# Optimization experiments

Measured on AMD Instinct MI355X. Metric: run time of the kernel, lower is better.

Reference implementation:

```python
import jax, jax.numpy as jnp
import numpy as np

D_MODEL, D_K, D_V, H = 1024, 64, 64, 16
B, NQ, NK = 4, 1024, 1024
HID = D_MODEL // 2


def _dwg(x, W1, b1, W2, b2):
    # DynamicWeightGenerator: sigmoid(fc2(relu(fc1(x))))
    h = jax.nn.relu(jnp.einsum('bnd,hd->bnh', x, W1) + b1)
    return jax.nn.sigmoid(jnp.einsum('bnh,dh->bnd', h, W2) + b2)


def setup_inputs() -> dict:
    key = jax.random.key(0)
    ks = jax.random.split(key, 32)
    s = 0.02
    inp = {
        'queries': jax.random.normal(ks[0], (B, NQ, D_MODEL), jnp.float32),
        'keys': jax.random.normal(ks[1], (B, NK, D_MODEL), jnp.float32),
        'values': jax.random.normal(ks[2], (B, NK, D_MODEL), jnp.float32),
        'attention_mask': jax.random.randint(ks[3], (B, 1, NQ, NK), 0, 2) > 0,
        'attention_weights': jax.random.uniform(ks[4], (B, H, NQ, NK), jnp.float32),
        'memory': jax.random.normal(ks[5], (B, NK), jnp.float32),
        # projections (torch Linear convention: y = x @ W.T + b)
        'Wq': jax.random.normal(ks[6], (H * D_K, D_MODEL), jnp.float32) * s,
        'bq': jnp.zeros((H * D_K,), jnp.float32),
        'Wk': jax.random.normal(ks[7], (H * D_K, D_MODEL), jnp.float32) * s,
        'bk': jnp.zeros((H * D_K,), jnp.float32),
        'Wv': jax.random.normal(ks[8], (H * D_V, D_MODEL), jnp.float32) * s,
        'bv': jnp.zeros((H * D_V,), jnp.float32),
        'Wo': jax.random.normal(ks[9], (D_MODEL, H * D_V), jnp.float32) * s,
        'bo': jnp.zeros((D_MODEL,), jnp.float32),
        'Wmm': jax.random.normal(ks[10], (H * D_V, 1), jnp.float32) * s,
        'bmm': jnp.zeros((H * D_V,), jnp.float32),
    }
    for i, tag in enumerate(['q', 'k', 'v']):
        k0, k1 = ks[11 + 2 * i], ks[12 + 2 * i]
        inp[f'W1{tag}'] = jax.random.normal(k0, (HID, D_MODEL), jnp.float32) * s
        inp[f'b1{tag}'] = jnp.zeros((HID,), jnp.float32)
        inp[f'W2{tag}'] = jax.random.normal(k1, (D_MODEL, HID), jnp.float32) * s
        inp[f'b2{tag}'] = jnp.zeros((D_MODEL,), jnp.float32)
    return inp


def reference(queries, keys, values, attention_mask, attention_weights, memory,
              Wq, bq, Wk, bk, Wv, bv, Wo, bo, Wmm, bmm,
              W1q, b1q, W2q, b2q, W1k, b1k, W2k, b2k, W1v, b1v, W2v, b2v):
    b_s, nq = queries.shape[:2]
    nk = keys.shape[1]
    # dynamic elementwise gating of inputs
    q_in = queries * _dwg(queries, W1q, b1q, W2q, b2q)
    k_in = keys * _dwg(keys, W1k, b1k, W2k, b2k)
    v_in = values * _dwg(values, W1v, b1v, W2v, b2v)
    # projections -> (b, h, n, d)
    q = (jnp.einsum('bnd,ed->bne', q_in, Wq) + bq).reshape(b_s, nq, H, D_K).transpose(0, 2, 1, 3)
    k = (jnp.einsum('bnd,ed->bne', k_in, Wk) + bk).reshape(b_s, nk, H, D_K).transpose(0, 2, 1, 3)
    v = (jnp.einsum('bnd,ed->bne', v_in, Wv) + bv).reshape(b_s, nk, H, D_V).transpose(0, 2, 1, 3)
    # per-token memory factor: fc_mm(memory[..., None]) -> (b, h, nk, d_k)
    mm = (memory[..., None] * Wmm[:, 0] + bmm).reshape(b_s, nk, H, D_K).transpose(0, 2, 1, 3)
    att = jnp.einsum('bhqd,bhkd->bhqk', q, k * mm) / np.sqrt(D_K).astype(np.float32)
    att = att * attention_weights                         # custom scaling (slice [:nk] == full)
    att = jnp.where(attention_mask, -jnp.inf, att)        # masked_fill
    att = jax.nn.softmax(att, axis=-1)
    out = jnp.einsum('bhqk,bhkd->bhqd', att, v * mm)      # (b, h, nq, d_v)
    out = out.transpose(0, 2, 1, 3).reshape(b_s, nq, H * D_V)
    return jnp.einsum('bne,de->bnd', out, Wo) + bo
```

## Files before the change

### kernel.cpp

```cpp
#include <hip/hip_runtime.h>
#include <hip/hip_bf16.h>

#define BB    4
#define NN    1024
#define DM    1024
#define HH    16
#define HID   512
#define TT    (BB * NN)

typedef __attribute__((ext_vector_type(8))) short bf16x8;
typedef __attribute__((ext_vector_type(4))) float f32x4;

__device__ __forceinline__ ushort f2bfu(float f) {
    __hip_bfloat16 h = __float2bfloat16(f);
    return __builtin_bit_cast(ushort, h);
}

__device__ __forceinline__ float bfu2f(ushort u) {
    __hip_bfloat16 h = __builtin_bit_cast(__hip_bfloat16, u);
    return __bfloat162float(h);
}

__device__ __forceinline__ f32x4 mfma16(bf16x8 a, bf16x8 b, f32x4 c) {
    return __builtin_amdgcn_mfma_f32_16x16x32_bf16(a, b, c, 0, 0, 0);
}

__device__ __forceinline__ void gll16(const void* g, void* l) {
    __builtin_amdgcn_global_load_lds(
        (const __attribute__((address_space(1))) unsigned int*)g,
        (__attribute__((address_space(3))) unsigned int*)l, 16, 0, 0);
}

__global__ void detect_mask_kernel(const uint4* __restrict__ m,
                                   int n16, int* __restrict__ flags) {
    int stride = blockDim.x * gridDim.x;
    unsigned hi = 0, lo = 0;
    for (int i = blockIdx.x * blockDim.x + threadIdx.x; i < n16; i += stride) {
        uint4 v = m[i];
        unsigned o = v.x | v.y | v.z | v.w;
        lo |= o & 0xFFu;
        hi |= o & 0xFFFFFF00u;
    }
    if (hi) atomicOr(&flags[0], 1);
    if (lo) atomicOr(&flags[1], 1);
}

#define NSEG 13
struct CvtAll { const float* s[NSEG]; ushort* d[NSEG]; int bound[NSEG]; };

__global__ __launch_bounds__(256) void cvt_all(CvtAll a, int total) {
    int stride = blockDim.x * gridDim.x;
    for (int i = blockIdx.x * blockDim.x + threadIdx.x; i < total; i += stride) {
        const float* sp = a.s[0];
        ushort* dp = a.d[0];
        int base = 0;
        #pragma unroll
        for (int k = 1; k < NSEG; ++k) {
            bool ge = i >= a.bound[k - 1];
            sp = ge ? a.s[k] : sp;
            dp = ge ? a.d[k] : dp;
            base = ge ? a.bound[k - 1] : base;
        }
        int j = i - base;
        float4 v = ((const float4*)sp)[j];
        uint2 o;
        o.x = (unsigned)f2bfu(v.x) | ((unsigned)f2bfu(v.y) << 16);
        o.y = (unsigned)f2bfu(v.z) | ((unsigned)f2bfu(v.w) << 16);
        ((uint2*)dp)[j] = o;
    }
}

struct GB {
    const ushort* A[3]; const ushort* W[3];
    const float* bias[3]; void* C[3]; const ushort* X[3];
};

template <int EP, int NF>
__global__ __launch_bounds__(256) void gemm_bf16(
    GB gb, int M, int N, int K,
    const float* __restrict__ mem, const float* __restrict__ Wmm,
    const float* __restrict__ bmm)
{
    __shared__ __align__(16) ushort As[2][128 * 64];
    __shared__ __align__(16) ushort Bs[2][NF * 32 * 64];
    const int z = blockIdx.z;
    const ushort* A = gb.A[z];
    const ushort* W = gb.W[z];
    const float* bias = gb.bias[z];
    void* Cout = gb.C[z];
    const ushort* X = gb.X[z];

    const int tid = threadIdx.x;
    const int lane = tid & 63, w = tid >> 6;
    const int lc = lane & 15, lg = lane >> 4;
    const int m0 = blockIdx.x * 128, n0 = blockIdx.y * (NF * 32);
    const int wm = (w >> 1) * 64, wn = (w & 1) * (NF * 16);
    const int srow = lane >> 3, scol = 8 * ((lane & 7) ^ srow);
    const int swl = (lc & 7) << 3;

    f32x4 acc[4][NF];
    #pragma unroll
    for (int i = 0; i < 4; ++i)
        #pragma unroll
        for (int j = 0; j < NF; ++j)
            acc[i][j] = (f32x4){0.f, 0.f, 0.f, 0.f};

    auto stage = [&](int buf, int k0) {
        #pragma unroll
        for (int ci = 0; ci < 4; ++ci) {
            int c = w + ci * 4;
            gll16(&A[(size_t)(m0 + c * 8 + srow) * K + k0 + scol], &As[buf][c * 512]);
            if (c < NF * 4)
                gll16(&W[(size_t)(n0 + c * 8 + srow) * K + k0 + scol], &Bs[buf][c * 512]);
        }
    };

    stage(0, 0);
    stage(1, 64);
    const int nt = K / 64;

    for (int t = 0; t < nt; ++t) {
        const int cur = t & 1;
        if (t < nt - 1) {
            if constexpr (NF == 4) asm volatile("s_waitcnt vmcnt(8)" ::: "memory");
            else                   asm volatile("s_waitcnt vmcnt(6)" ::: "memory");
        } else {
            asm volatile("s_waitcnt vmcnt(0)" ::: "memory");
        }
        __builtin_amdgcn_sched_barrier(0);
        __builtin_amdgcn_s_barrier();

        bf16x8 af[4][2], bfr[NF][2];
        #pragma unroll
        for (int mi = 0; mi < 4; ++mi) {
            int row = wm + mi * 16 + lc;
            af[mi][0] = *(const bf16x8*)&As[cur][row * 64 + ((lg * 8) ^ swl)];
            af[mi][1] = *(const bf16x8*)&As[cur][row * 64 + ((32 + lg * 8) ^ swl)];
        }
        #pragma unroll
        for (int nj = 0; nj < NF; ++nj) {
            int row = wn + nj * 16 + lc;
            bfr[nj][0] = *(const bf16x8*)&Bs[cur][row * 64 + ((lg * 8) ^ swl)];
            bfr[nj][1] = *(const bf16x8*)&Bs[cur][row * 64 + ((32 + lg * 8) ^ swl)];
        }
        asm volatile("s_waitcnt lgkmcnt(0)" ::: "memory");
        __builtin_amdgcn_sched_barrier(0);
        __builtin_amdgcn_s_barrier();

        if (t + 2 < nt) stage(cur, (t + 2) * 64);

        #pragma unroll
        for (int mi = 0; mi < 4; ++mi)
            #pragma unroll
            for (int nj = 0; nj < NF; ++nj) {
                acc[mi][nj] = mfma16(af[mi][0], bfr[nj][0], acc[mi][nj]);
                acc[mi][nj] = mfma16(af[mi][1], bfr[nj][1], acc[mi][nj]);
            }
    }

    #pragma unroll
    for (int nj = 0; nj < NF; ++nj) {
        int e = n0 + wn + nj * 16 + lc;
        float bv = bias[e];
        float wmv = 0.f, bmv = 0.f;
        if (EP == 7) { wmv = Wmm[e]; bmv = bmm[e]; }
        #pragma unroll
        for (int mi = 0; mi < 4; ++mi) {
            int mbase = m0 + wm + mi * 16 + lg * 4;
            if (EP == 7 && z == 2) {
                ushort u[4];
                #pragma unroll
                for (int r = 0; r < 4; ++r) {
                    float v = (acc[mi][nj][r] + bv) * (mem[mbase + r] * wmv + bmv);
                    u[r] = f2bfu(v);
                }
                int bb = mbase >> 10, n = mbase & 1023;
                size_t off = ((size_t)(bb * HH + (e >> 6)) * 64 + (e & 63)) * NN + n;
                uint2 pk;
                pk.x = (unsigned)u[0] | ((unsigned)u[1] << 16);
                pk.y = (unsigned)u[2] | ((unsigned)u[3] << 16);
                *(uint2*)&((ushort*)Cout)[off] = pk;
            } else {
                #pragma unroll
                for (int r = 0; r < 4; ++r) {
                    int m = mbase + r;
                    float v = acc[mi][nj][r] + bv;
                    if (EP == 1) v = fmaxf(v, 0.f);
                    if (EP == 2) v = bfu2f(X[(size_t)m * N + e]) * (1.f / (1.f + __expf(-v)));
                    if (EP == 7) {
                        if (z == 0) v = v * 0.125f;
                        else        v = v * (mem[m] * wmv + bmv);
                    }
                    size_t off = (size_t)m * N + e;
                    if (EP == 4) ((float*)Cout)[off] = v;
                    else         ((ushort*)Cout)[off] = f2bfu(v);
                }
            }
        }
    }
}

__global__ __launch_bounds__(256) void attn_mfma(
    const ushort* __restrict__ qp, const ushort* __restrict__ kp,
    const ushort* __restrict__ vt, const float* __restrict__ aw,
    const void* __restrict__ maskp, const int* __restrict__ mflags,
    ushort* __restrict__ ob)
{
    __shared__ __align__(16) ushort Ks[2][64 * 64];
    __shared__ __align__(16) ushort Vs[2][64 * 64];
    __shared__ __align__(16) ushort Ps[64 * 64];
    const int tid = threadIdx.x, lane = tid & 63, w = tid >> 6;
    const int lc = lane & 15, lg = lane >> 4;
    const int bid = blockIdx.x;
    const int swz = (bid & 7) * 128 + (bid >> 3);
    const int qt = swz & 15, bh = swz >> 4;
    const int b = bh >> 4, h = bh & 15;
    const int q0 = qt * 64, wq = w * 16;
    const int mode = mflags[0] ? (mflags[1] ? 1 : 2) : 0;
    const int srow = lane >> 3, scol = 8 * ((lane & 7) ^ srow);
    const int swl = (lc & 7) << 3;

    const ushort* qrow = &qp[(size_t)(b * NN + q0 + wq + lc) * DM + h * 64];
    bf16x8 bq0 = *(const bf16x8*)&qrow[lg * 8];
    bf16x8 bq1 = *(const bf16x8*)&qrow[32 + lg * 8];

    f32x4 oacc[4];
    #pragma unroll
    for (int i = 0; i < 4; ++i) oacc[i] = (f32x4){0.f, 0.f, 0.f, 0.f};
    float psum = 0.f;
    const int q = q0 + wq + lc;
    const float* awrow = aw + ((size_t)bh * NN + q) * NN;
    const size_t mrowo = ((size_t)b * NN + q) * NN;

    float4 awA[4], awB[4];
    uint4 mk4A[4], mk4B[4];
    unsigned mk1A[4], mk1B[4];

    #pragma unroll
    for (int ci = 0; ci < 2; ++ci) {
        int c = w + ci * 4;
        gll16(&kp[(size_t)(b * NN + c * 8 + srow) * DM + h * 64 + scol], &Ks[0][c * 512]);
        gll16(&vt[((size_t)bh * 64 + c * 8 + srow) * NN + 0 + scol], &Vs[0][c * 512]);
    }
    #pragma unroll
    for (int mi = 0; mi < 4; ++mi)
        awA[mi] = *(const float4*)&awrow[mi * 16 + lg * 4];
    if (mode == 1) {
        #pragma unroll
        for (int mi = 0; mi < 4; ++mi)
            mk1A[mi] = *(const unsigned*)&((const unsigned char*)maskp)[mrowo + mi * 16 + lg * 4];
    } else {
        #pragma unroll
        for (int mi = 0; mi < 4; ++mi)
            mk4A[mi] = *(const uint4*)((const char*)maskp + 4 * (mrowo + mi * 16 + lg * 4));
    }
    asm volatile("s_waitcnt vmcnt(0)" ::: "memory");
    __builtin_amdgcn_sched_barrier(0);
    __builtin_amdgcn_s_barrier();

#define ATTN_BODY(T, AWC, MK4C, MK1C, AWN, MK4N, MK1N)                          \
    {                                                                           \
        const int cur = (T) & 1;                                                \
        if ((T) < 15) {                                                         \
            const int kn = ((T) + 1) * 64;                                      \
            _Pragma("unroll")                                                   \
            for (int ci = 0; ci < 2; ++ci) {                                    \
                int c = w + ci * 4;                                             \
                gll16(&kp[(size_t)(b * NN + kn + c * 8 + srow) * DM + h * 64 + scol], \
                      &Ks[cur ^ 1][c * 512]);                                   \
                gll16(&vt[((size_t)bh * 64 + c * 8 + srow) * NN + kn + scol],   \
                      &Vs[cur ^ 1][c * 512]);                                   \
            }                                                                   \
            __builtin_amdgcn_sched_barrier(0);                                  \
            _Pragma("unroll")                                                   \
            for (int mi = 0; mi < 4; ++mi)                                      \
                AWN[mi] = *(const float4*)&awrow[kn + mi * 16 + lg * 4];        \
            if (mode == 1) {                                                    \
                _Pragma("unroll")                                               \
                for (int mi = 0; mi < 4; ++mi)                                  \
                    MK1N[mi] = *(const unsigned*)&((const unsigned char*)maskp) \
                                   [mrowo + kn + mi * 16 + lg * 4];             \
            } else {                                                            \
                _Pragma("unroll")                                               \
                for (int mi = 0; mi < 4; ++mi)                                  \
                    MK4N[mi] = *(const uint4*)((const char*)maskp +             \
                                   4 * (mrowo + kn + mi * 16 + lg * 4));        \
            }                                                                   \
            __builtin_amdgcn_sched_barrier(0);                                  \
        }                                                                       \
                                                               \
        f32x4 sacc[4];                                                          \
        __builtin_amdgcn_s_setprio(1);                                          \
        _Pragma("unroll")                                                       \
        for (int mi = 0; mi < 4; ++mi) {                                        \
            int krow = mi * 16 + lc;                                            \
            bf16x8 a0 = *(const bf16x8*)&Ks[cur][krow * 64 + ((lg * 8) ^ swl)]; \
            bf16x8 a1 = *(const bf16x8*)&Ks[cur][krow * 64 + ((32 + lg * 8) ^ swl)]; \
            f32x4 s = (f32x4){0.f, 0.f, 0.f, 0.f};                              \
            s = mfma16(a0, bq0, s);                                             \
            s = mfma16(a1, bq1, s);                                             \
            sacc[mi] = s;                                                       \
        }                                                                       \
        __builtin_amdgcn_s_setprio(0);                                          \
                                 \
        _Pragma("unroll")                                                       \
        for (int mi = 0; mi < 4; ++mi) {                                        \
            unsigned mk[4];                                                     \
            if (mode == 1) {                                                    \
                mk[0] = MK1C[mi] & 0xffu;         mk[1] = (MK1C[mi] >> 8) & 0xffu;  \
                mk[2] = (MK1C[mi] >> 16) & 0xffu; mk[3] = (MK1C[mi] >> 24) & 0xffu; \
            } else if (mode == 0) {                                             \
                mk[0] = MK4C[mi].x; mk[1] = MK4C[mi].y;                         \
                mk[2] = MK4C[mi].z; mk[3] = MK4C[mi].w;                         \
            } else {                                                            \
                mk[0] = MK4C[mi].x != 0; mk[1] = MK4C[mi].y != 0;               \
                mk[2] = MK4C[mi].z != 0; mk[3] = MK4C[mi].w != 0;               \
            }                                                                   \
            const float aww[4] = {AWC[mi].x, AWC[mi].y, AWC[mi].z, AWC[mi].w};  \
            float pv[4];                                                        \
            _Pragma("unroll")                                                   \
            for (int r = 0; r < 4; ++r) {                                       \
                float sv = sacc[mi][r] * aww[r];                                \
                pv[r] = mk[r] ? 0.f : __expf(sv);                               \
                psum += pv[r];                                                  \
            }                                                                   \
            uint2 pk;                                                           \
            pk.x = (unsigned)f2bfu(pv[0]) | ((unsigned)f2bfu(pv[1]) << 16);     \
            pk.y = (unsigned)f2bfu(pv[2]) | ((unsigned)f2bfu(pv[3]) << 16);     \
            *(uint2*)&Ps[(wq + lc) * 64 + ((mi * 16 + lg * 4) ^ swl)] = pk;     \
        }                                                                       \
                                                                        \
        __builtin_amdgcn_s_setprio(1);                                          \
        _Pragma("unroll")                                                       \
        for (int kk = 0; kk < 2; ++kk) {                                        \
            bf16x8 pa = *(const bf16x8*)&Ps[(wq + lc) * 64 + ((kk * 32 + lg * 8) ^ swl)]; \
            _Pragma("unroll")                                                   \
            for (int nj = 0; nj < 4; ++nj) {                                    \
                bf16x8 vb = *(const bf16x8*)&Vs[cur][(nj * 16 + lc) * 64 + ((kk * 32 + lg * 8) ^ swl)]; \
                oacc[nj] = mfma16(pa, vb, oacc[nj]);                            \
            }                                                                   \
        }                                                                       \
        __builtin_amdgcn_s_setprio(0);                                          \
        if ((T) < 15) {                                                         \
            asm volatile("s_waitcnt vmcnt(0)" ::: "memory");                    \
            __builtin_amdgcn_sched_barrier(0);                                  \
            __builtin_amdgcn_s_barrier();                                       \
        }                                                                       \
    }

    for (int tt = 0; tt < 8; ++tt) {
        const int t0 = tt * 2, t1 = tt * 2 + 1;
        ATTN_BODY(t0, awA, mk4A, mk1A, awB, mk4B, mk1B);
        ATTN_BODY(t1, awB, mk4B, mk1B, awA, mk4A, mk1A);
    }
#undef ATTN_BODY

    psum += __shfl_xor(psum, 16);
    psum += __shfl_xor(psum, 32);
    float inv = 1.0f / psum;
    float invr[4];
    #pragma unroll
    for (int r = 0; r < 4; ++r)
        invr[r] = __shfl(inv, (lane & 48) | (lg * 4 + r));

    #pragma unroll
    for (int nj = 0; nj < 4; ++nj)
        #pragma unroll
        for (int r = 0; r < 4; ++r) {
            int qq = q0 + wq + lg * 4 + r;
            float v = oacc[nj][r] * invr[r];
            ob[(size_t)(b * NN + qq) * DM + h * 64 + nj * 16 + lc] = f2bfu(v);
        }
}

extern "C" void kernel_launch(void* const* d_in, const int* in_sizes, int n_in,
                              void* d_out, int out_size, void* d_ws, size_t ws_size,
                              hipStream_t stream) {
    const float* xin_f[3] = {(const float*)d_in[0], (const float*)d_in[1], (const float*)d_in[2]};
    const void*  maskp   = d_in[3];
    const float* aw      = (const float*)d_in[4];
    const float* memv    = (const float*)d_in[5];
    const float* Wp_f[3] = {(const float*)d_in[6], (const float*)d_in[8], (const float*)d_in[10]};
    const float* bp[3]   = {(const float*)d_in[7], (const float*)d_in[9], (const float*)d_in[11]};
    const float* Wo_f  = (const float*)d_in[12];  const float* bo  = (const float*)d_in[13];
    const float* Wmm = (const float*)d_in[14];    const float* bmm = (const float*)d_in[15];
    const float* W1f[3] = {(const float*)d_in[16], (const float*)d_in[20], (const float*)d_in[24]};
    const float* b1a[3] = {(const float*)d_in[17], (const float*)d_in[21], (const float*)d_in[25]};
    const float* W2f[3] = {(const float*)d_in[18], (const float*)d_in[22], (const float*)d_in[26]};
    const float* b2a[3] = {(const float*)d_in[19], (const float*)d_in[23], (const float*)d_in[27]};

    char* p = (char*)d_ws;
    auto alloc = [&](size_t bytes) { char* r = p; p += (bytes + 255) & ~(size_t)255; return r; };
    int*    mflags = (int*)alloc(256);
    ushort* xbf[3]; for (int t = 0; t < 3; ++t) xbf[t] = (ushort*)alloc((size_t)TT * DM * 2);
    ushort* Wpb[3]; for (int t = 0; t < 3; ++t) Wpb[t] = (ushort*)alloc((size_t)DM * DM * 2);
    ushort* Wob  = (ushort*)alloc((size_t)DM * DM * 2);
    ushort* W1b[3]; for (int t = 0; t < 3; ++t) W1b[t] = (ushort*)alloc((size_t)HID * DM * 2);
    ushort* W2b[3]; for (int t = 0; t < 3; ++t) W2b[t] = (ushort*)alloc((size_t)DM * HID * 2);
    ushort* hbuf[3]; for (int t = 0; t < 3; ++t) hbuf[t] = (ushort*)alloc((size_t)TT * HID * 2);
    ushort* xg[3];  for (int t = 0; t < 3; ++t) xg[t] = (ushort*)alloc((size_t)TT * DM * 2);
    ushort* qpb  = (ushort*)alloc((size_t)TT * DM * 2);
    ushort* ksb  = (ushort*)alloc((size_t)TT * DM * 2);
    ushort* vtb  = (ushort*)alloc((size_t)TT * DM * 2);
    ushort* obuf = (ushort*)alloc((size_t)TT * DM * 2);

    hipMemsetAsync(mflags, 0, 8, stream);
    detect_mask_kernel<<<256, 256, 0, stream>>>((const uint4*)maskp,
                                                BB * NN * NN / 16, mflags);

    {
        CvtAll a;
        const int S_IN = TT * DM / 4, S_W = DM * DM / 4, S_H = HID * DM / 4;
        int idx = 0, cum = 0;
        auto seg = [&](const float* s, ushort* d, int n) {
            a.s[idx] = s; a.d[idx] = d; cum += n; a.bound[idx] = cum; ++idx;
        };
        for (int t = 0; t < 3; ++t) seg(xin_f[t], xbf[t], S_IN);
        for (int t = 0; t < 3; ++t) seg(Wp_f[t], Wpb[t], S_W);
        seg(Wo_f, Wob, S_W);
        for (int t = 0; t < 3; ++t) seg(W1f[t], W1b[t], S_H);
        for (int t = 0; t < 3; ++t) seg(W2f[t], W2b[t], S_H);
        cvt_all<<<2048, 256, 0, stream>>>(a, cum);
    }

    const dim3 blk(256);
    GB g1 = {}, g2 = {}, g3 = {}, g4 = {};
    for (int t = 0; t < 3; ++t) {
        g1.A[t] = xbf[t];  g1.W[t] = W1b[t]; g1.bias[t] = b1a[t]; g1.C[t] = hbuf[t];
        g2.A[t] = hbuf[t]; g2.W[t] = W2b[t]; g2.bias[t] = b2a[t]; g2.C[t] = xg[t]; g2.X[t] = xbf[t];
        g3.A[t] = xg[t];   g3.W[t] = Wpb[t]; g3.bias[t] = bp[t];
    }
    g3.C[0] = qpb; g3.C[1] = ksb; g3.C[2] = vtb;
    g4.A[0] = obuf; g4.W[0] = Wob; g4.bias[0] = bo; g4.C[0] = d_out;

    gemm_bf16<1, 2><<<dim3(TT / 128, HID / 64, 3), blk, 0, stream>>>(g1, TT, HID, DM, nullptr, nullptr, nullptr);
    gemm_bf16<2, 2><<<dim3(TT / 128, DM / 64, 3), blk, 0, stream>>>(g2, TT, DM, HID, nullptr, nullptr, nullptr);
    gemm_bf16<7, 2><<<dim3(TT / 128, DM / 64, 3), blk, 0, stream>>>(g3, TT, DM, DM, memv, Wmm, bmm);

    attn_mfma<<<dim3(1024), blk, 0, stream>>>(qpb, ksb, vtb, aw,
                                              maskp, mflags, obuf);

    gemm_bf16<4, 2><<<dim3(TT / 128, DM / 64, 1), blk, 0, stream>>>(g4, TT, DM, DM, nullptr, nullptr, nullptr);
}
```

Before: 260.9 us.

## Add LDS-staged triple-use attention kernel with async prefetch of weights and mask

Measured after the change: 269.0 us. +3.1%, slower.

```diff
diff --git a/kernel.cpp b/kernel.cpp
--- a/kernel.cpp
+++ b/kernel.cpp
@@ -200,12 +200,176 @@
     }
 }
 
-__global__ __launch_bounds__(256) void attn_mfma(
+__global__ __launch_bounds__(256) void attn_fast(
+    const ushort* __restrict__ qp, const ushort* __restrict__ kp,
+    const ushort* __restrict__ vt, const float* __restrict__ aw,
+    const unsigned char* __restrict__ maskp, const int* __restrict__ mflags,
+    ushort* __restrict__ ob)
+{
+    const int mode = mflags[0] ? (mflags[1] ? 1 : 2) : 0;
+    if (mode != 1) return;
+
+    __shared__ __align__(16) ushort Ks[2][64 * 64];
+    __shared__ __align__(16) ushort Vs[2][64 * 64];
+    __shared__ __align__(16) float  AWs[2][64 * 64];
+    __shared__ __align__(16) unsigned char Ms[2][64 * 64];
+    __shared__ __align__(16) ushort Ps[64 * 64];
+
+    const int tid = threadIdx.x, lane = tid & 63, w = tid >> 6;
+    const int lc = lane & 15, lg = lane >> 4;
+    const int bid = blockIdx.x;
+    const int swz = (bid & 7) * 128 + (bid >> 3);
+    const int qt = swz & 15, bh = swz >> 4;
+    const int b = bh >> 4, h = bh & 15;
+    const int q0 = qt * 64, wq = w * 16;
+    const int srow = lane >> 3, scol = 8 * ((lane & 7) ^ srow);
+    const int swl = (lc & 7) << 3;
+    const int qloc = wq + lc;
+
+    const ushort* qrow = &qp[(size_t)(b * NN + q0 + qloc) * DM + h * 64];
+    bf16x8 bq0 = *(const bf16x8*)&qrow[lg * 8];
+    bf16x8 bq1 = *(const bf16x8*)&qrow[32 + lg * 8];
+
+    auto stage = [&](int buf, int t) {
+        const int k0 = t * 64;
+        #pragma unroll
+        for (int ci = 0; ci < 2; ++ci) {
+            int c = w + ci * 4;
+            gll16(&kp[(size_t)(b * NN + k0 + c * 8 + srow) * DM + h * 64 + scol],
+                  &Ks[buf][c * 512]);
+            gll16(&vt[((size_t)bh * 64 + c * 8 + srow) * NN + k0 + scol],
+                  &Vs[buf][c * 512]);
+        }
+        #pragma unroll
+        for (int ci = 0; ci < 4; ++ci) {
+            int c = w + ci * 4;
+            int row = c * 4 + (lane >> 4);
+            int un = (lane & 15) ^ (row & 7);
+            gll16(&aw[((size_t)bh * NN + q0 + row) * NN + k0 + un * 4],
+                  &AWs[buf][c * 256]);
+        }
+        {
+            int row = w * 16 + (lane >> 2);
+            int un = (lane & 3) ^ (row & 3);
+            gll16(&maskp[((size_t)b * NN + q0 + row) * NN + k0 + un * 16],
+                  &Ms[buf][w * 1024]);
+        }
+    };
+
+    f32x4 oacc[4];
+    #pragma unroll
+    for (int i = 0; i < 4; ++i) oacc[i] = (f32x4){0.f, 0.f, 0.f, 0.f};
+    float psum = 0.f;
+
+    stage(0, 0);
+    stage(1, 1);
+    asm volatile("s_waitcnt vmcnt(0)" ::: "memory");
+    __builtin_amdgcn_sched_barrier(0);
+    __builtin_amdgcn_s_barrier();
+
+    const int awk = qloc & 7;
+    const int mkk = qloc & 3;
+
+    for (int t = 0; t < 16; ++t) {
+        const int cur = t & 1;
+        if (t < 15) asm volatile("s_waitcnt vmcnt(9)" ::: "memory");
+        else        asm volatile("s_waitcnt vmcnt(0)" ::: "memory");
+        __builtin_amdgcn_sched_barrier(0);
+        __builtin_amdgcn_s_barrier();
+
+        bf16x8 af0[4], af1[4], vf0[4], vf1[4];
+        float4 awf[4];
+        unsigned mkf[4];
+        #pragma unroll
+        for (int mi = 0; mi < 4; ++mi) {
+            int krow = mi * 16 + lc;
+            af0[mi] = *(const bf16x8*)&Ks[cur][krow * 64 + ((lg * 8) ^ swl)];
+            af1[mi] = *(const bf16x8*)&Ks[cur][krow * 64 + ((32 + lg * 8) ^ swl)];
+        }
+        #pragma unroll
+        for (int nj = 0; nj < 4; ++nj) {
+            int vrow = nj * 16 + lc;
+            vf0[nj] = *(const bf16x8*)&Vs[cur][vrow * 64 + ((lg * 8) ^ swl)];
+            vf1[nj] = *(const bf16x8*)&Vs[cur][vrow * 64 + ((32 + lg * 8) ^ swl)];
+        }
+        #pragma unroll
+        for (int mi = 0; mi < 4; ++mi) {
+            awf[mi] = *(const float4*)&AWs[cur][qloc * 64 + (((mi * 4 + lg) ^ awk) * 4)];
+            mkf[mi] = *(const unsigned*)&Ms[cur][qloc * 64 + ((mi ^ mkk) * 16) + lg * 4];
+        }
+        asm volatile("s_waitcnt lgkmcnt(0)" ::: "memory");
+        __builtin_amdgcn_sched_barrier(0);
+        __builtin_amdgcn_s_barrier();
+
+        if (t + 2 < 16) stage(cur, t + 2);
+
+        f32x4 sacc[4];
+        __builtin_amdgcn_s_setprio(1);
+        #pragma unroll
+        for (int mi = 0; mi < 4; ++mi) {
+            f32x4 s = (f32x4){0.f, 0.f, 0.f, 0.f};
+            s = mfma16(af0[mi], bq0, s);
+            s = mfma16(af1[mi], bq1, s);
+            sacc[mi] = s;
+        }
+        __builtin_amdgcn_s_setprio(0);
+
+        #pragma unroll
+        for (int mi = 0; mi < 4; ++mi) {
+            unsigned mu = mkf[mi];
+            const float aww[4] = {awf[mi].x, awf[mi].y, awf[mi].z, awf[mi].w};
+            float pv[4];
+            pv[0] = (mu & 0xffu)         ? 0.f : __expf(sacc[mi][0] * aww[0]);
+            pv[1] = ((mu >> 8) & 0xffu)  ? 0.f : __expf(sacc[mi][1] * aww[1]);
+            pv[2] = ((mu >> 16) & 0xffu) ? 0.f : __expf(sacc[mi][2] * aww[2]);
+            pv[3] = ((mu >> 24) & 0xffu) ? 0.f : __expf(sacc[mi][3] * aww[3]);
+            psum += pv[0] + pv[1] + pv[2] + pv[3];
+            uint2 pk;
+            pk.x = (unsigned)f2bfu(pv[0]) | ((unsigned)f2bfu(pv[1]) << 16);
+            pk.y = (unsigned)f2bfu(pv[2]) | ((unsigned)f2bfu(pv[3]) << 16);
+            *(uint2*)&Ps[qloc * 64 + ((mi * 16 + lg * 4) ^ swl)] = pk;
+        }
+
+        __builtin_amdgcn_s_setprio(1);
+        {
+            bf16x8 pa0 = *(const bf16x8*)&Ps[qloc * 64 + ((lg * 8) ^ swl)];
+            #pragma unroll
+            for (int nj = 0; nj < 4; ++nj)
+                oacc[nj] = mfma16(pa0, vf0[nj], oacc[nj]);
+            bf16x8 pa1 = *(const bf16x8*)&Ps[qloc * 64 + ((32 + lg * 8) ^ swl)];
+            #pragma unroll
+            for (int nj = 0; nj < 4; ++nj)
+                oacc[nj] = mfma16(pa1, vf1[nj], oacc[nj]);
+        }
+        __builtin_amdgcn_s_setprio(0);
+    }
+
+    psum += __shfl_xor(psum, 16);
+    psum += __shfl_xor(psum, 32);
+    float inv = 1.0f / psum;
+    float invr[4];
+    #pragma unroll
+    for (int r = 0; r < 4; ++r)
+        invr[r] = __shfl(inv, (lane & 48) | (lg * 4 + r));
+
+    #pragma unroll
+    for (int nj = 0; nj < 4; ++nj)
+        #pragma unroll
+        for (int r = 0; r < 4; ++r) {
+            int qq = q0 + wq + lg * 4 + r;
+            float v = oacc[nj][r] * invr[r];
+            ob[(size_t)(b * NN + qq) * DM + h * 64 + nj * 16 + lc] = f2bfu(v);
+        }
+}
+
+__global__ __launch_bounds__(256) void attn_mfma_fb(
     const ushort* __restrict__ qp, const ushort* __restrict__ kp,
     const ushort* __restrict__ vt, const float* __restrict__ aw,
     const void* __restrict__ maskp, const int* __restrict__ mflags,
     ushort* __restrict__ ob)
 {
+    const int mode = mflags[0] ? (mflags[1] ? 1 : 2) : 0;
+    if (mode == 1) return;
     __shared__ __align__(16) ushort Ks[2][64 * 64];
     __shared__ __align__(16) ushort Vs[2][64 * 64];
     __shared__ __align__(16) ushort Ps[64 * 64];
@@ -216,7 +380,6 @@
     const int qt = swz & 15, bh = swz >> 4;
     const int b = bh >> 4, h = bh & 15;
     const int q0 = qt * 64, wq = w * 16;
-    const int mode = mflags[0] ? (mflags[1] ? 1 : 2) : 0;
     const int srow = lane >> 3, scol = 8 * ((lane & 7) ^ srow);
     const int swl = (lc & 7) << 3;
 
@@ -234,7 +397,6 @@
 
     float4 awA[4], awB[4];
     uint4 mk4A[4], mk4B[4];
-    unsigned mk1A[4], mk1B[4];
 
     #pragma unroll
     for (int ci = 0; ci < 2; ++ci) {
@@ -243,22 +405,15 @@
         gll16(&vt[((size_t)bh * 64 + c * 8 + srow) * NN + 0 + scol], &Vs[0][c * 512]);
     }
     #pragma unroll
-    for (int mi = 0; mi < 4; ++mi)
+    for (int mi = 0; mi < 4; ++mi) {
         awA[mi] = *(const float4*)&awrow[mi * 16 + lg * 4];
-    if (mode == 1) {
-        #pragma unroll
-        for (int mi = 0; mi < 4; ++mi)
-            mk1A[mi] = *(const unsigned*)&((const unsigned char*)maskp)[mrowo + mi * 16 + lg * 4];
-    } else {
-        #pragma unroll
-        for (int mi = 0; mi < 4; ++mi)
-            mk4A[mi] = *(const uint4*)((const char*)maskp + 4 * (mrowo + mi * 16 + lg * 4));
+        mk4A[mi] = *(const uint4*)((const char*)maskp + 4 * (mrowo + mi * 16 + lg * 4));
     }
     asm volatile("s_waitcnt vmcnt(0)" ::: "memory");
     __builtin_amdgcn_sched_barrier(0);
     __builtin_amdgcn_s_barrier();
 
-#define ATTN_BODY(T, AWC, MK4C, MK1C, AWN, MK4N, MK1N)                          \
+#define ATTN_BODY(T, AWC, MK4C, AWN, MK4N)                                      \
     {                                                                           \
         const int cur = (T) & 1;                                                \
         if ((T) < 15) {                                                         \
@@ -273,22 +428,13 @@
             }                                                                   \
             __builtin_amdgcn_sched_barrier(0);                                  \
             _Pragma("unroll")                                                   \
-            for (int mi = 0; mi < 4; ++mi)                                      \
+            for (int mi = 0; mi < 4; ++mi) {                                    \
                 AWN[mi] = *(const float4*)&awrow[kn + mi * 16 + lg * 4];        \
-            if (mode == 1) {                                                    \
-                _Pragma("unroll")                                               \
-                for (int mi = 0; mi < 4; ++mi)                                  \
-                    MK1N[mi] = *(const unsigned*)&((const unsigned char*)maskp) \
-                                   [mrowo + kn + mi * 16 + lg * 4];             \
-            } else {                                                            \
-                _Pragma("unroll")                                               \
-                for (int mi = 0; mi < 4; ++mi)                                  \
-                    MK4N[mi] = *(const uint4*)((const char*)maskp +             \
-                                   4 * (mrowo + kn + mi * 16 + lg * 4));        \
+                MK4N[mi] = *(const uint4*)((const char*)maskp +                 \
+                               4 * (mrowo + kn + mi * 16 + lg * 4));            \
             }                                                                   \
             __builtin_amdgcn_sched_barrier(0);                                  \
         }                                                                       \
-                                                               \
         f32x4 sacc[4];                                                          \
         __builtin_amdgcn_s_setprio(1);                                          \
         _Pragma("unroll")                                                       \
@@ -302,14 +448,10 @@
             sacc[mi] = s;                                                       \
         }                                                                       \
         __builtin_amdgcn_s_setprio(0);                                          \
-                                 \
         _Pragma("unroll")                                                       \
         for (int mi = 0; mi < 4; ++mi) {                                        \
             unsigned mk[4];                                                     \
-            if (mode == 1) {                                                    \
-                mk[0] = MK1C[mi] & 0xffu;         mk[1] = (MK1C[mi] >> 8) & 0xffu;  \
-                mk[2] = (MK1C[mi] >> 16) & 0xffu; mk[3] = (MK1C[mi] >> 24) & 0xffu; \
-            } else if (mode == 0) {                                             \
+            if (mode == 0) {                                                    \
                 mk[0] = MK4C[mi].x; mk[1] = MK4C[mi].y;                         \
                 mk[2] = MK4C[mi].z; mk[3] = MK4C[mi].w;                         \
             } else {                                                            \
@@ -329,7 +471,6 @@
             pk.y = (unsigned)f2bfu(pv[2]) | ((unsigned)f2bfu(pv[3]) << 16);     \
             *(uint2*)&Ps[(wq + lc) * 64 + ((mi * 16 + lg * 4) ^ swl)] = pk;     \
         }                                                                       \
-                                                                        \
         __builtin_amdgcn_s_setprio(1);                                          \
         _Pragma("unroll")                                                       \
         for (int kk = 0; kk < 2; ++kk) {                                        \
@@ -350,8 +491,8 @@
 
     for (int tt = 0; tt < 8; ++tt) {
         const int t0 = tt * 2, t1 = tt * 2 + 1;
-        ATTN_BODY(t0, awA, mk4A, mk1A, awB, mk4B, mk1B);
-        ATTN_BODY(t1, awB, mk4B, mk1B, awA, mk4A, mk1A);
+        ATTN_BODY(t0, awA, mk4A, awB, mk4B);
+        ATTN_BODY(t1, awB, mk4B, awA, mk4A);
     }
 #undef ATTN_BODY
 
@@ -437,8 +578,10 @@
     gemm_bf16<2, 2><<<dim3(TT / 128, DM / 64, 3), blk, 0, stream>>>(g2, TT, DM, HID, nullptr, nullptr, nullptr);
     gemm_bf16<7, 2><<<dim3(TT / 128, DM / 64, 3), blk, 0, stream>>>(g3, TT, DM, DM, memv, Wmm, bmm);
 
-    attn_mfma<<<dim3(1024), blk, 0, stream>>>(qpb, ksb, vtb, aw,
-                                              maskp, mflags, obuf);
+    attn_fast<<<dim3(1024), blk, 0, stream>>>(qpb, ksb, vtb, aw,
+                                              (const unsigned char*)maskp, mflags, obuf);
+    attn_mfma_fb<<<dim3(1024), blk, 0, stream>>>(qpb, ksb, vtb, aw,
+                                                 maskp, mflags, obuf);
 
     gemm_bf16<4, 2><<<dim3(TT / 128, DM / 64, 1), blk, 0, stream>>>(g4, TT, DM, DM, nullptr, nullptr, nullptr);
 }
```
